# Performance work log

Hardware: AMD Instinct MI355X
Metric: run time of the kernel (lower is better)

The kernel has to match this reference:

```python
import jax, jax.numpy as jnp
import numpy as np

N_HOS, N_TYP, N_STRUCTS = 2, 3, 8
N_COMBOS = N_HOS * N_TYP  # 6
BATCH = 32768
N_ITERS = 150  # PDHG iterations to solve the per-sample QP

S_NP = np.array([[1,0,0,1,0,1,0,0],
                 [0,1,0,1,0,0,1,0],
                 [0,0,1,0,1,0,0,1],
                 [1,0,0,0,1,1,0,0],
                 [0,1,0,0,0,0,1,1],
                 [0,0,1,1,1,0,0,0]], dtype=np.float32)


def setup_inputs() -> dict:
    key = jax.random.key(0)
    ks = jax.random.split(key, 10)
    def lin(kw, fan_in, fan_out):
        lim = 1.0 / np.sqrt(fan_in)
        kw1, kw2 = jax.random.split(kw)
        W = jax.random.uniform(kw1, (fan_out, fan_in), jnp.float32, -lim, lim)
        b = jax.random.uniform(kw2, (fan_out,), jnp.float32, -lim, lim)
        return W, b
    W1, b1 = lin(ks[0], 6, 20)
    W2, b2 = lin(ks[1], 20, 20)
    W3, b3 = lin(ks[2], 20, 20)
    W4, b4 = lin(ks[3], 20, 8)
    X = jax.random.uniform(ks[4], (BATCH, N_HOS, N_TYP), jnp.float32)  # nonneg bids -> feasible QP (x=0)
    return {"X": X, "W1": W1, "b1": b1, "W2": W2, "b2": b2, "W3": W3, "b3": b3,
            "W4": W4, "b4": b4, "S": jnp.asarray(S_NP), "batch_size": BATCH}


def _solve_qp(z, b, S):
    """Batched PDHG for: max w.x - ||x-z||_2  s.t. x>=0, S x <= b, with w = 1.
    z: [B, ns], b: [B, m], S: [m, ns]. Returns x: [B, ns]."""
    B, ns = z.shape
    m = S.shape[0]
    w = jnp.ones_like(z)
    # K = [S; -I]; Frobenius bound on spectral norm (safe step sizes)
    L = jnp.sqrt(jnp.sum(S * S) + ns)
    tau = 0.9 / L
    sigma = 0.9 / L

    def prox_f(u):
        # prox of tau*(||x-z|| - w.x) at u  (closed form: shifted norm shrinkage)
        v = u + tau * w - z
        nv = jnp.linalg.norm(v, axis=-1, keepdims=True)
        scale = jnp.maximum(1.0 - tau / jnp.maximum(nv, 1e-12), 0.0)
        return z + scale * v

    def step(carry, _):
        x, l1, l2 = carry
        x_new = prox_f(x - tau * (l1 @ S - l2))  # K^T lam = S^T l1 - l2
        xbar = 2.0 * x_new - x
        l1n = jnp.maximum(l1 + sigma * (xbar @ S.T) - sigma * b, 0.0)  # dual of Sx<=b
        l2n = jnp.maximum(l2 - sigma * xbar, 0.0)                      # dual of -x<=0
        return (x_new, l1n, l2n), None

    x0 = jnp.maximum(z, 0.0)
    l1 = jnp.zeros((B, m), z.dtype)
    l2 = jnp.zeros((B, ns), z.dtype)
    (x, _, _), _ = jax.lax.scan(step, (x0, l1, l2), None, length=N_ITERS)
    return x


def reference(X, W1, b1, W2, b2, W3, b3, W4, b4, S, batch_size):
    B = X.shape[0]
    Z = X.reshape(B, -1)                       # [B, 6] = bids flattened (also the QP rhs b)
    h = jnp.tanh(Z @ W1.T + b1)
    h = jnp.tanh(h @ W2.T + b2)
    h = jnp.tanh(h @ W3.T + b3)
    z = jnp.tanh(h @ W4.T + b4)                # [B, 8] anchor point for QP
    return _solve_qp(z, Z, S)                  # [B, 8] allocation
```

## Files before the change

### kernel.cpp

```cpp
#include <hip/hip_runtime.h>
#include <math.h>


#define NITERS 150

__device__ __forceinline__ float ftanh(float a) {
    float e = __expf(2.0f * a);
    return fmaf(-2.0f, __builtin_amdgcn_rcpf(e + 1.0f), 1.0f);
}

template<int P0, int P1, int P2, int P3>
__device__ __forceinline__ float qp(float x) {
    constexpr int ctrl = P0 | (P1 << 2) | (P2 << 4) | (P3 << 6);
    int xi = __builtin_bit_cast(int, x);
    int yi = __builtin_amdgcn_update_dpp(0, xi, ctrl, 0xF, 0xF, true);
    return __builtin_bit_cast(float, yi);
}

#define FOR20(M) M(0) M(1) M(2) M(3) M(4) M(5) M(6) M(7) M(8) M(9) \
                 M(10) M(11) M(12) M(13) M(14) M(15) M(16) M(17) M(18) M(19)
#define FOR8(M)  M(0) M(1) M(2) M(3) M(4) M(5) M(6) M(7)

#define DOT20(W, base, H) \
  ( (fmaf(W[(base)+0],H##0,  fmaf(W[(base)+1],H##1,  fmaf(W[(base)+2],H##2,  fmaf(W[(base)+3],H##3,  W[(base)+4]*H##4)))) \
   + fmaf(W[(base)+5],H##5,  fmaf(W[(base)+6],H##6,  fmaf(W[(base)+7],H##7,  fmaf(W[(base)+8],H##8,  W[(base)+9]*H##9))))) \
  + (fmaf(W[(base)+10],H##10, fmaf(W[(base)+11],H##11, fmaf(W[(base)+12],H##12, fmaf(W[(base)+13],H##13, W[(base)+14]*H##14)))) \
   + fmaf(W[(base)+15],H##15, fmaf(W[(base)+16],H##16, fmaf(W[(base)+17],H##17, fmaf(W[(base)+18],H##18, W[(base)+19]*H##19))))) )

#define DOT6(W, base, P) \
  ( fmaf(W[(base)+0],P##0, fmaf(W[(base)+1],P##1, W[(base)+2]*P##2)) \
  + fmaf(W[(base)+3],P##3, fmaf(W[(base)+4],P##4, W[(base)+5]*P##5)) )

__global__ __launch_bounds__(256, 2)
void matchnet_kernel(
    const float* __restrict__ X,
    const float* __restrict__ W1, const float* __restrict__ b1,
    const float* __restrict__ W2, const float* __restrict__ b2,
    const float* __restrict__ W3, const float* __restrict__ b3,
    const float* __restrict__ W4, const float* __restrict__ b4,
    float* __restrict__ out, int B)
{
    const int tid = blockIdx.x * 256 + threadIdx.x;
    const int s   = tid >> 2;
    if (s >= B) return;
    const int g   = tid & 3;

    const float TAU = 0.9f / sqrtf(26.0f);
    const float SIG = TAU;
    const float TS  = TAU * SIG;

    float zin0, zin1, zin2, zin3, zin4, zin5;
    {
        const float2* xp = (const float2*)(X + (size_t)s * 6);
        float2 p0 = xp[0], p1 = xp[1], p2 = xp[2];
        zin0 = p0.x; zin1 = p0.y; zin2 = p1.x;
        zin3 = p1.y; zin4 = p2.x; zin5 = p2.y;
    }

#define L1ROW(j) float h1_##j = ftanh(b1[j] + DOT6(W1, (j)*6, zin));
    FOR20(L1ROW)
#define L2ROW(j) float h2_##j = ftanh(b2[j] + DOT20(W2, (j)*20, h1_));
    FOR20(L2ROW)
#define L3ROW(j) float h3_##j = ftanh(b3[j] + DOT20(W3, (j)*20, h2_));
    FOR20(L3ROW)
#define ZROW(j)  float z##j  = ftanh(b4[j] + DOT20(W4, (j)*20, h3_));
    FOR8(ZROW)

    const bool b0 = (g & 1), b1_ = (g & 2);
    float z01 = b0 ? z1 : z0,  z23 = b0 ? z3 : z2;
    float zA  = b1_ ? z23 : z01;
    float z45 = b0 ? z5 : z4,  z67 = b0 ? z7 : z6;
    float zB  = b1_ ? z67 : z45;

    float i01 = b0 ? zin1 : zin0, i23 = b0 ? zin3 : zin2;
    float igA = b1_ ? i23 : i01;
    float i45 = b0 ? zin5 : zin4;
    float sbA = SIG * igA;
    float sbB = (g < 2) ? SIG * i45 : 1e30f;

    float zptA = zA + TAU, zptB = zB + TAU;
    float xzA  = fmaxf(zA, 0.0f) - zA + TAU;
    float xzB  = fmaxf(zB, 0.0f) - zB + TAU;
    float qA = 0.0f, qB = 0.0f;
    float pA = xzA,  pB = xzB;
    float lA = 0.0f, lB = 0.0f;

    const bool sel03 = (g == 0) || (g == 3);
    const bool sel01 = (g < 2);
    const bool sel1  = (g == 1);

#pragma unroll 1
    for (int it = 0; it < NITERS; ++it) {
        float gA1  = qp<0,1,2,0>(lA);
        float gA2a = qp<3,0,0,1>(lA);
        float gA2b = qp<0,0,1,0>(lB);
        float gA2  = sel03 ? gA2a : gA2b;
        float gA3  = qp<2,2,2,1>(lB);
        float stA = (gA1 + gA2) + gA3;
        float gB1  = qp<2,0,1,2>(lA);
        float gB2a = qp<3,3,0,0>(lA);
        float gB2b = qp<0,0,0,0>(lB);
        float gB2  = sel01 ? gB2a : gB2b;
        float gB3  = qp<1,2,2,2>(lB);
        float stB = (gB1 + gB2) + gB3;

        float vA = fmaf(-TAU, stA, pA);
        float vB = fmaf(-TAU, stB, pB);

        float nl = fmaf(vA, vA, vB * vB);
        nl = nl + qp<1,0,3,2>(nl);
        nl = nl + qp<2,3,0,1>(nl);
        float scale = fmaxf(fmaf(-TAU, __builtin_amdgcn_rsqf(nl), 1.0f), 0.0f);
        float ss2 = scale + scale;

        float xbA = fmaf(ss2, vA, zptA - xzA);
        float xbB = fmaf(ss2, vB, zptB - xzB);
        xzA = fmaf(scale, vA, TAU);
        xzB = fmaf(scale, vB, TAU);
        qA  = fmaxf(fmaf(-TS, xbA, qA), 0.0f);
        qB  = fmaxf(fmaf(-TS, xbB, qB), 0.0f);
        pA  = xzA + qA;
        pB  = xzB + qB;

        float h1  = qp<0,1,2,0>(xbA);
        float h2a = qp<3,3,0,0>(xbA);
        float h2b = qp<0,0,0,0>(xbB);
        float h2  = sel01 ? h2a : h2b;
        float h3  = qp<1,2,3,1>(xbB);
        float rA = (h1 + h2) + h3;
        float k1  = qp<1,2,0,0>(xbA);
        float k2a = qp<0,3,0,0>(xbA);
        float k2b = qp<2,0,0,0>(xbB);
        float k2  = sel1 ? k2a : k2b;
        float k3  = qp<3,0,0,0>(xbB);
        float rB = (k1 + k2) + k3;

        lA = fmaxf(fmaf(SIG, rA, lA) - sbA, 0.0f);
        lB = fmaxf(fmaf(SIG, rB, lB) - sbB, 0.0f);
    }

    const float T2 = 2.0f * TAU;
    out[(size_t)s * 8 + g]     = xzA + zptA - T2;
    out[(size_t)s * 8 + 4 + g] = xzB + zptB - T2;
}

extern "C" void kernel_launch(void* const* d_in, const int* in_sizes, int n_in,
                              void* d_out, int out_size, void* d_ws, size_t ws_size,
                              hipStream_t stream) {
    const float* X  = (const float*)d_in[0];
    const float* W1 = (const float*)d_in[1];
    const float* b1 = (const float*)d_in[2];
    const float* W2 = (const float*)d_in[3];
    const float* b2 = (const float*)d_in[4];
    const float* W3 = (const float*)d_in[5];
    const float* b3 = (const float*)d_in[6];
    const float* W4 = (const float*)d_in[7];
    const float* b4 = (const float*)d_in[8];
    float* out = (float*)d_out;
    const int B = in_sizes[0] / 6;
    const int threads = B * 4;
    const int blocks = (threads + 255) / 256;
    hipLaunchKernelGGL(matchnet_kernel, dim3(blocks), dim3(256), 0, stream,
                       X, W1, b1, W2, b2, W3, b3, W4, b4, out, B);
}
```

Before: 114.6 us.

## Use packed float2 math for MLP layers and PDHG state updates

Rewrites the MLP dot products as two-wide vector FMAs over paired hidden activations, which can map to packed FP32 instructions (v_pk_fma_f32) on CDNA. The PDHG loop's A/B primal state is rearranged into v2 vectors and reformulated around w = z - scale*v, removing the separate xz and zpt variables and some scalar ops. It also adds horizontal reductions per row, packing and unpacking moves, and possible register pressure.

```diff
diff --git a/kernel.cpp b/kernel.cpp
--- a/kernel.cpp
+++ b/kernel.cpp
@@ -3,6 +3,16 @@
 
 
 #define NITERS 150
+
+typedef float v2 __attribute__((ext_vector_type(2)));
+
+__device__ __forceinline__ v2 vfma(v2 a, v2 b, v2 c) {
+    return __builtin_elementwise_fma(a, b, c);
+}
+__device__ __forceinline__ v2 vmax(v2 a, v2 b) {
+    return __builtin_elementwise_max(a, b);
+}
+#define LD2(W, off) (*(const v2*)((W) + (off)))
 
 __device__ __forceinline__ float ftanh(float a) {
     float e = __expf(2.0f * a);
@@ -21,15 +31,17 @@
                  M(10) M(11) M(12) M(13) M(14) M(15) M(16) M(17) M(18) M(19)
 #define FOR8(M)  M(0) M(1) M(2) M(3) M(4) M(5) M(6) M(7)
 
-#define DOT20(W, base, H) \
-  ( (fmaf(W[(base)+0],H##0,  fmaf(W[(base)+1],H##1,  fmaf(W[(base)+2],H##2,  fmaf(W[(base)+3],H##3,  W[(base)+4]*H##4)))) \
-   + fmaf(W[(base)+5],H##5,  fmaf(W[(base)+6],H##6,  fmaf(W[(base)+7],H##7,  fmaf(W[(base)+8],H##8,  W[(base)+9]*H##9))))) \
-  + (fmaf(W[(base)+10],H##10, fmaf(W[(base)+11],H##11, fmaf(W[(base)+12],H##12, fmaf(W[(base)+13],H##13, W[(base)+14]*H##14)))) \
-   + fmaf(W[(base)+15],H##15, fmaf(W[(base)+16],H##16, fmaf(W[(base)+17],H##17, fmaf(W[(base)+18],H##18, W[(base)+19]*H##19))))) )
+#define PK20(W, base, H) \
+  ( vfma(LD2(W,(base)+0),H##0, vfma(LD2(W,(base)+4),H##2, vfma(LD2(W,(base)+8),H##4, \
+      vfma(LD2(W,(base)+12),H##6, LD2(W,(base)+16)*H##8)))) \
+  + vfma(LD2(W,(base)+2),H##1, vfma(LD2(W,(base)+6),H##3, vfma(LD2(W,(base)+10),H##5, \
+      vfma(LD2(W,(base)+14),H##7, LD2(W,(base)+18)*H##9)))) )
 
-#define DOT6(W, base, P) \
-  ( fmaf(W[(base)+0],P##0, fmaf(W[(base)+1],P##1, W[(base)+2]*P##2)) \
-  + fmaf(W[(base)+3],P##3, fmaf(W[(base)+4],P##4, W[(base)+5]*P##5)) )
+#define PACK10(P, t) \
+  v2 P##0 = {t##_0,  t##_1},  P##1 = {t##_2,  t##_3},  P##2 = {t##_4,  t##_5}; \
+  v2 P##3 = {t##_6,  t##_7},  P##4 = {t##_8,  t##_9},  P##5 = {t##_10, t##_11}; \
+  v2 P##6 = {t##_12, t##_13}, P##7 = {t##_14, t##_15}, P##8 = {t##_16, t##_17}; \
+  v2 P##9 = {t##_18, t##_19};
 
 __global__ __launch_bounds__(256, 2)
 void matchnet_kernel(
@@ -50,21 +62,34 @@
     const float TS  = TAU * SIG;
 
     float zin0, zin1, zin2, zin3, zin4, zin5;
+    v2 zin01, zin23, zin45;
     {
         const float2* xp = (const float2*)(X + (size_t)s * 6);
         float2 p0 = xp[0], p1 = xp[1], p2 = xp[2];
         zin0 = p0.x; zin1 = p0.y; zin2 = p1.x;
         zin3 = p1.y; zin4 = p2.x; zin5 = p2.y;
+        zin01 = (v2){p0.x, p0.y}; zin23 = (v2){p1.x, p1.y}; zin45 = (v2){p2.x, p2.y};
     }
 
-#define L1ROW(j) float h1_##j = ftanh(b1[j] + DOT6(W1, (j)*6, zin));
-    FOR20(L1ROW)
-#define L2ROW(j) float h2_##j = ftanh(b2[j] + DOT20(W2, (j)*20, h1_));
-    FOR20(L2ROW)
-#define L3ROW(j) float h3_##j = ftanh(b3[j] + DOT20(W3, (j)*20, h2_));
-    FOR20(L3ROW)
-#define ZROW(j)  float z##j  = ftanh(b4[j] + DOT20(W4, (j)*20, h3_));
-    FOR8(ZROW)
+#define L1R(j) float t1_##j; { \
+        v2 r_ = vfma(LD2(W1,(j)*6+0), zin01, vfma(LD2(W1,(j)*6+2), zin23, LD2(W1,(j)*6+4)*zin45)); \
+        t1_##j = ftanh(b1[j] + (r_.x + r_.y)); }
+    FOR20(L1R)
+    PACK10(A, t1)
+#define L2R(j) float t2_##j; { \
+        v2 r_ = PK20(W2, (j)*20, A); \
+        t2_##j = ftanh(b2[j] + (r_.x + r_.y)); }
+    FOR20(L2R)
+    PACK10(Bh, t2)
+#define L3R(j) float t3_##j; { \
+        v2 r_ = PK20(W3, (j)*20, Bh); \
+        t3_##j = ftanh(b3[j] + (r_.x + r_.y)); }
+    FOR20(L3R)
+    PACK10(C, t3)
+#define ZR(j) float z##j; { \
+        v2 r_ = PK20(W4, (j)*20, C); \
+        z##j = ftanh(b4[j] + (r_.x + r_.y)); }
+    FOR8(ZR)
 
     const bool b0 = (g & 1), b1_ = (g & 2);
     float z01 = b0 ? z1 : z0,  z23 = b0 ? z3 : z2;
@@ -78,60 +103,61 @@
     float sbA = SIG * igA;
     float sbB = (g < 2) ? SIG * i45 : 1e30f;
 
-    float zptA = zA + TAU, zptB = zB + TAU;
-    float xzA  = fmaxf(zA, 0.0f) - zA + TAU;
-    float xzB  = fmaxf(zB, 0.0f) - zB + TAU;
-    float qA = 0.0f, qB = 0.0f;
-    float pA = xzA,  pB = xzB;
+    v2 zv = {zA, zB};
+    v2 w  = {zA + zA - fmaxf(zA, 0.0f), zB + zB - fmaxf(zB, 0.0f)};
+    v2 q  = {0.0f, 0.0f};
+    v2 p  = {fmaxf(-zA, 0.0f) + TAU, fmaxf(-zB, 0.0f) + TAU};
     float lA = 0.0f, lB = 0.0f;
 
-    const bool sel03 = (g == 0) || (g == 3);
-    const bool sel01 = (g < 2);
-    const bool sel1  = (g == 1);
+    const v2 vTAU  = {TAU, TAU};
+    const v2 vmTAU = {-TAU, -TAU};
+    const v2 vmTS  = {-TS, -TS};
+    const v2 vTWO  = {2.0f, 2.0f};
+    const v2 vZERO = {0.0f, 0.0f};
 
 #pragma unroll 1
     for (int it = 0; it < NITERS; ++it) {
         float gA1  = qp<0,1,2,0>(lA);
         float gA2a = qp<3,0,0,1>(lA);
         float gA2b = qp<0,0,1,0>(lB);
-        float gA2  = sel03 ? gA2a : gA2b;
+        float gA2  = ((g == 0) || (g == 3)) ? gA2a : gA2b;
         float gA3  = qp<2,2,2,1>(lB);
         float stA = (gA1 + gA2) + gA3;
         float gB1  = qp<2,0,1,2>(lA);
         float gB2a = qp<3,3,0,0>(lA);
         float gB2b = qp<0,0,0,0>(lB);
-        float gB2  = sel01 ? gB2a : gB2b;
+        float gB2  = (g < 2) ? gB2a : gB2b;
         float gB3  = qp<1,2,2,2>(lB);
         float stB = (gB1 + gB2) + gB3;
 
-        float vA = fmaf(-TAU, stA, pA);
-        float vB = fmaf(-TAU, stB, pB);
+        v2 st = {stA, stB};
+        v2 v  = vfma(vmTAU, st, p);
 
-        float nl = fmaf(vA, vA, vB * vB);
+        v2 sq = v * v;
+        float nl = sq.x + sq.y;
         nl = nl + qp<1,0,3,2>(nl);
         nl = nl + qp<2,3,0,1>(nl);
         float scale = fmaxf(fmaf(-TAU, __builtin_amdgcn_rsqf(nl), 1.0f), 0.0f);
-        float ss2 = scale + scale;
+        v2 vscale = {scale, scale};
 
-        float xbA = fmaf(ss2, vA, zptA - xzA);
-        float xbB = fmaf(ss2, vB, zptB - xzB);
-        xzA = fmaf(scale, vA, TAU);
-        xzB = fmaf(scale, vB, TAU);
-        qA  = fmaxf(fmaf(-TS, xbA, qA), 0.0f);
-        qB  = fmaxf(fmaf(-TS, xbB, qB), 0.0f);
-        pA  = xzA + qA;
-        pB  = xzB + qB;
+        v2 sv = vscale * v;
+        v2 xb = vfma(vTWO, sv, w);
+        w = zv - sv;
+        q = vmax(vfma(vmTS, xb, q), vZERO);
+        p = (sv + q) + vTAU;
+
+        float xbA = xb.x, xbB = xb.y;
 
         float h1  = qp<0,1,2,0>(xbA);
         float h2a = qp<3,3,0,0>(xbA);
         float h2b = qp<0,0,0,0>(xbB);
-        float h2  = sel01 ? h2a : h2b;
+        float h2  = (g < 2) ? h2a : h2b;
         float h3  = qp<1,2,3,1>(xbB);
         float rA = (h1 + h2) + h3;
         float k1  = qp<1,2,0,0>(xbA);
         float k2a = qp<0,3,0,0>(xbA);
         float k2b = qp<2,0,0,0>(xbB);
-        float k2  = sel1 ? k2a : k2b;
+        float k2  = (g == 1) ? k2a : k2b;
         float k3  = qp<3,0,0,0>(xbB);
         float rB = (k1 + k2) + k3;
 
@@ -139,9 +165,8 @@
         lB = fmaxf(fmaf(SIG, rB, lB) - sbB, 0.0f);
     }
 
-    const float T2 = 2.0f * TAU;
-    out[(size_t)s * 8 + g]     = xzA + zptA - T2;
-    out[(size_t)s * 8 + 4 + g] = xzB + zptB - T2;
+    out[(size_t)s * 8 + g]     = zA + zA - w.x;
+    out[(size_t)s * 8 + 4 + g] = zB + zB - w.y;
 }
 
 extern "C" void kernel_launch(void* const* d_in, const int* in_sizes, int n_in,
```

Measured after the change: 111.5 us. -2.7%, faster.
